# Kernel optimization log

Hardware: AMD Instinct MI355X
Metric: run time of the kernel (lower is better)

## Reference

```python
import jax, jax.numpy as jnp
import numpy as np

NUM_HEADS = 8
BLOCK_SIZE = 32   # tokens per block
WINDOW = 64       # window radius in blocks -> attends to blocks [i-64, i+64]


def setup_inputs() -> dict:
    key = jax.random.key(0)
    ks = jax.random.split(key, 5)
    B, N, C = 8, 8192, 512
    s = 0.02
    return {
        "x": jax.random.normal(ks[0], (B, N, C), dtype=jnp.float32),
        # torch Linear(dim, 3*dim): y = x @ W.T + b; we store W already transposed [in, out]
        "W_qkv": jax.random.normal(ks[1], (C, 3 * C), dtype=jnp.float32) * s,
        "b_qkv": jax.random.normal(ks[2], (3 * C,), dtype=jnp.float32) * s,
        "W_proj": jax.random.normal(ks[3], (C, C), dtype=jnp.float32) * s,
        "b_proj": jax.random.normal(ks[4], (C,), dtype=jnp.float32) * s,
    }


def reference(x, W_qkv, b_qkv, W_proj, b_proj):
    B, N, C = x.shape
    h = NUM_HEADS
    dh = C // h
    scale = jnp.asarray(dh, x.dtype) ** -0.5

    # qkv projection, then the module's head-interleaved split:
    # rearrange 'b n (h d) -> b h n d' with d = 3C/h, chunk(3) on last dim,
    # rearrange back 'b h n d -> b n (h d)'. Equivalent to:
    qkv = (x @ W_qkv + b_qkv).reshape(B, N, h, 3 * dh)
    q = qkv[..., :dh].reshape(B, N, C)
    k = qkv[..., dh:2 * dh].reshape(B, N, C)
    v = qkv[..., 2 * dh:].reshape(B, N, C)

    # dynamic blocking (N chosen divisible by BLOCK_SIZE -> no padding)
    nb = N // BLOCK_SIZE
    qb = q.reshape(B, nb, BLOCK_SIZE, C)
    kb = k.reshape(B, nb, BLOCK_SIZE, C)
    vb = v.reshape(B, nb, BLOCK_SIZE, C)

    # per-offset block attention: query block i, position s attends to
    # position s of every block j in [i-WINDOW, i+WINDOW]
    attn = jnp.einsum('bisc,bjsc->bisj', qb, kb) * scale  # [B, nb, s, nb]
    i_idx = jnp.arange(nb)[:, None]
    j_idx = jnp.arange(nb)[None, :]
    band = (j_idx >= i_idx - WINDOW) & (j_idx <= i_idx + WINDOW)  # [nb, nb]
    neg = jnp.finfo(attn.dtype).min
    attn = jnp.where(band[None, :, None, :], attn, neg)
    attn = jax.nn.softmax(attn, axis=-1)
    out = jnp.einsum('bisj,bjsc->bisc', attn, vb)  # [B, nb, s, C]
    out = out.reshape(B, N, C)

    # 'b n (h d) -> b n h d -> b n (h d)' is the identity
    return out @ W_proj + b_proj
```

## Files before the change

kernel.cpp:

```cpp
#include <hip/hip_runtime.h>
#include <hip/hip_bf16.h>
#include <stdint.h>

#define B_   8
#define N_   8192
#define C_   512
#define NB   256
#define WIN  64

typedef __attribute__((ext_vector_type(8))) short short8;
typedef __attribute__((ext_vector_type(4))) float f32x4;
typedef __hip_bfloat16 bf16;

__device__ __forceinline__ void gload_lds16(const void* g, void* l) {
  __builtin_amdgcn_global_load_lds((const __attribute__((address_space(1))) void*)g,
                                   (__attribute__((address_space(3))) void*)l, 16, 0, 0);
}

__device__ __forceinline__ f32x4 mfma16(short8 a, short8 b, f32x4 c) {
  return __builtin_amdgcn_mfma_f32_16x16x32_bf16(a, b, c, 0, 0, 0);
}


__global__ __launch_bounds__(256) void k_conv_x(const float4* __restrict__ x,
                                                ushort4* __restrict__ xb) {
  size_t idx = (size_t)blockIdx.x * 256 + threadIdx.x;
  float4 v = x[idx];
  union { ushort4 u; bf16 b[4]; } o;
  o.b[0] = __float2bfloat16(v.x); o.b[1] = __float2bfloat16(v.y);
  o.b[2] = __float2bfloat16(v.z); o.b[3] = __float2bfloat16(v.w);
  xb[idx] = o.u;
}

__global__ __launch_bounds__(256) void k_conv_wqkv(const float* __restrict__ W,
                                                   const float* __restrict__ bq,
                                                   bf16* __restrict__ Wt,
                                                   float* __restrict__ bperm) {
  int o = blockIdx.x;
  int part = o >> 9;
  int c = o & 511;
  int h = c >> 6, d = c & 63;
  int src = h * 192 + part * 64 + d;
  for (int kk = threadIdx.x; kk < 512; kk += 256)
    Wt[(size_t)o * 512 + kk] = __float2bfloat16(W[(size_t)kk * 1536 + src]);
  if (threadIdx.x == 0) bperm[o] = bq[src];
}

__global__ __launch_bounds__(256) void k_conv_wproj(const float* __restrict__ W,
                                                    bf16* __restrict__ Wt) {
  int o = blockIdx.x;
  for (int kk = threadIdx.x; kk < 512; kk += 256)
    Wt[(size_t)o * 512 + kk] = __float2bfloat16(W[(size_t)kk * 512 + o]);
}

template <int EPI>
__global__ __launch_bounds__(512, 2) void k_gemm(const bf16* __restrict__ A,
                                                 const bf16* __restrict__ Bt,
                                                 const float* __restrict__ bias,
                                                 bf16* __restrict__ qb,
                                                 bf16* __restrict__ kb,
                                                 bf16* __restrict__ vb,
                                                 float* __restrict__ outf,
                                                 int NT) {
  extern __shared__ bf16 sm[];
  const int tid = threadIdx.x;
  const int lane = tid & 63, wid = tid >> 6;
  const int wr = wid >> 2, wcn = wid & 3;
  const int l15 = lane & 15, l4 = lane >> 4;

  const int nwg = gridDim.x;
  const int cpx = nwg >> 3;
  const int swz = (blockIdx.x & 7) * cpx + (blockIdx.x >> 3);
  const int mt = swz / NT, nt = swz % NT;
  const size_t m0 = (size_t)mt * 256;
  const int n0 = nt * 256;

  f32x4 acc[8][4];
#pragma unroll
  for (int fi = 0; fi < 8; ++fi)
#pragma unroll
    for (int fj = 0; fj < 4; ++fj) acc[fi][fj] = (f32x4){0.f, 0.f, 0.f, 0.f};

#define STAGEG(slot, k0)                                                       \
  {                                                                            \
    bf16* Adst = sm + (slot) * 32768;                                          \
    bf16* Bdst = Adst + 16384;                                                 \
    _Pragma("unroll") for (int i = 0; i < 4; ++i) {                            \
      int li = i * 512 + tid;                                                  \
      int row = li >> 3, ch = li & 7;                                          \
      int chs = ch ^ (row & 7);                                                \
      gload_lds16(A + (m0 + row) * 512 + (k0) + chs * 8,                       \
                  (char*)Adst + li * 16);                                      \
      gload_lds16(Bt + (size_t)(n0 + row) * 512 + (k0) + chs * 8,              \
                  (char*)Bdst + li * 16);                                      \
    }                                                                          \
  }

  STAGEG(0, 0);
  for (int t = 0; t < 8; ++t) {
    if (t < 7) {
      STAGEG((t + 1) & 1, (t + 1) * 64);
      asm volatile("s_waitcnt vmcnt(8)" ::: "memory");
    } else {
      asm volatile("s_waitcnt vmcnt(0)" ::: "memory");
    }
    __builtin_amdgcn_s_barrier();
    __builtin_amdgcn_sched_barrier(0);
    const bf16* Ap = sm + (t & 1) * 32768;
    const bf16* Bp = Ap + 16384;
#pragma unroll
    for (int ks = 0; ks < 2; ++ks) {
      short8 a[8], b[4];
#pragma unroll
      for (int fi = 0; fi < 8; ++fi) {
        int ra = wr * 128 + fi * 16 + l15;
        a[fi] = *(const short8*)&Ap[ra * 64 + (((ks * 4 + l4) ^ (ra & 7)) << 3)];
      }
#pragma unroll
      for (int fj = 0; fj < 4; ++fj) {
        int rb = wcn * 64 + fj * 16 + l15;
        b[fj] = *(const short8*)&Bp[rb * 64 + (((ks * 4 + l4) ^ (rb & 7)) << 3)];
      }
      __builtin_amdgcn_s_setprio(1);
#pragma unroll
      for (int fi = 0; fi < 8; ++fi)
#pragma unroll
        for (int fj = 0; fj < 4; ++fj)
          acc[fi][fj] = mfma16(a[fi], b[fj], acc[fi][fj]);
      __builtin_amdgcn_s_setprio(0);
    }
    __builtin_amdgcn_sched_barrier(0);
    __builtin_amdgcn_s_barrier();
  }
#undef STAGEG

  if (EPI == 0) {
#pragma unroll
    for (int fi = 0; fi < 8; ++fi)
#pragma unroll
      for (int fj = 0; fj < 4; ++fj) {
        int o = n0 + wcn * 64 + fj * 16 + l15;
        float bia = bias[o];
        int part = o >> 9;
        int c = o & 511;
        bf16* dst = part == 0 ? qb : (part == 1 ? kb : vb);
#pragma unroll
        for (int r = 0; r < 4; ++r) {
          size_t m = m0 + wr * 128 + fi * 16 + l4 * 4 + r;
          int bidx = (int)(m >> 13);
          int n = (int)(m & 8191);
          int blk = n >> 5, s = n & 31;
          size_t di = (((size_t)(bidx * 32 + s) * 256 + blk) << 9) | c;
          dst[di] = __float2bfloat16(acc[fi][fj][r] + bia);
        }
      }
  } else {
#pragma unroll
    for (int fi = 0; fi < 8; ++fi)
#pragma unroll
      for (int fj = 0; fj < 4; ++fj) {
        int o = n0 + wcn * 64 + fj * 16 + l15;
        float bia = bias[o];
#pragma unroll
        for (int r = 0; r < 4; ++r) {
          size_t m = m0 + wr * 128 + fi * 16 + l4 * 4 + r;
          outf[m * 512 + o] = acc[fi][fj][r] + bia;
        }
      }
  }
}

__global__ __launch_bounds__(256) void k_transpose_v(const bf16* __restrict__ v,
                                                     bf16* __restrict__ vT) {
  __shared__ bf16 t[32][36];
  int bs = blockIdx.x, j0 = blockIdx.y * 32, c0 = blockIdx.z * 32;
  const bf16* src = v + (size_t)bs * NB * C_;
  bf16* dst = vT + (size_t)bs * C_ * NB;
  int r = threadIdx.x >> 3, c4 = (threadIdx.x & 7) * 4;
  *(ushort4*)&t[r][c4] = *(const ushort4*)(src + (size_t)(j0 + r) * C_ + c0 + c4);
  __syncthreads();
  union { ushort4 u; bf16 b[4]; } o;
  o.b[0] = t[c4 + 0][r]; o.b[1] = t[c4 + 1][r];
  o.b[2] = t[c4 + 2][r]; o.b[3] = t[c4 + 3][r];
  *(ushort4*)(dst + (size_t)(c0 + r) * NB + j0 + c4) = o.u;
}

#define QS_OFF   0
#define KB_OFF   32768
#define VB_OFF   98304
#define SS_OFF   131072
#define PS_OFF   135296
#define SR_OFF   137856
#define MR_OFF   141952
#define LR_OFF   142080
#define AL_OFF   142208
#define ATTN_LDS 142336

__global__ __launch_bounds__(512) void k_attn(const bf16* __restrict__ qg,
                                              const bf16* __restrict__ kg,
                                              const bf16* __restrict__ vTg,
                                              bf16* __restrict__ outb) {
  extern __shared__ char smc[];
  float* Ssf  = (float*)(smc + SS_OFF);
  bf16*  Psb  = (bf16*)(smc + PS_OFF);
  float* Sred = (float*)(smc + SR_OFF);
  float* mrow = (float*)(smc + MR_OFF);
  float* lrow = (float*)(smc + LR_OFF);
  float* alph = (float*)(smc + AL_OFF);

  const int tid = threadIdx.x, lane = tid & 63, wid = tid >> 6;
  const int l15 = lane & 15, l4 = lane >> 4;
  const int gt = (blockIdx.x & 7) * 256 + (blockIdx.x >> 3);
  const int bs = gt >> 3;
  const int b = bs >> 5, s = bs & 31;
  const int i0 = (gt & 7) * 32;
  const int jlo = max(0, i0 - WIN);
  const int jhi = min(NB - 1, i0 + 31 + WIN);
  const int nch = (jhi - jlo + 1) >> 5;
  const bf16* Qb = qg + (size_t)bs * NB * C_;
  const bf16* Kb = kg + (size_t)bs * NB * C_;
  const bf16* Vb = vTg + (size_t)bs * C_ * NB;

  const int qh_qk = (wid >> 2) & 1, jh = (wid >> 1) & 1, ks = wid & 1;
  const int qh_pv = wid >> 2, cq = wid & 3;

  f32x4 O[8];
#pragma unroll
  for (int f = 0; f < 8; ++f) O[f] = (f32x4){0.f, 0.f, 0.f, 0.f};

  if (tid < 32) { mrow[tid] = -1e30f; lrow[tid] = 0.f; }

#pragma unroll
  for (int q = 0; q < 4; ++q) {
    int li = q * 512 + tid;
    int row = li >> 6, g = (li & 63) ^ (row & 15);
    gload_lds16(Qb + (size_t)(i0 + row) * C_ + g * 8, smc + QS_OFF + li * 16);
  }
#pragma unroll
  for (int q = 0; q < 4; ++q) {
    int li = q * 512 + tid;
    int row = li >> 6, g = (li & 63) ^ (row & 15);
    gload_lds16(Kb + (size_t)(jlo + row) * C_ + g * 8, smc + KB_OFF + li * 16);
  }

  for (int t = 0; t < nch; ++t) {
    const int j0 = jlo + t * 32;
    asm volatile("s_waitcnt vmcnt(0) lgkmcnt(0)" ::: "memory");
    __builtin_amdgcn_s_barrier();
    __builtin_amdgcn_sched_barrier(0);

#pragma unroll
    for (int q = 0; q < 4; ++q) {
      int li = q * 512 + tid;
      int c = li >> 2, g = (li & 3) ^ (c & 3);
      gload_lds16(Vb + (size_t)c * NB + j0 + g * 8, smc + VB_OFF + li * 16);
    }
    if (t + 1 < nch) {
      int jn = j0 + 32;
      char* kdst = smc + KB_OFF + ((t + 1) & 1) * 32768;
#pragma unroll
      for (int q = 0; q < 4; ++q) {
        int li = q * 512 + tid;
        int row = li >> 6, g = (li & 63) ^ (row & 15);
        gload_lds16(Kb + (size_t)(jn + row) * C_ + g * 8, kdst + li * 16);
      }
    }

    {
      const int arow = qh_qk * 16 + l15;
      const int brow = jh * 16 + l15;
      const char* Qbase = smc + QS_OFF + arow * 1024;
      const char* Kbase = smc + KB_OFF + (t & 1) * 32768 + brow * 1024;
      f32x4 a0 = (f32x4){0.f, 0.f, 0.f, 0.f}, a1 = a0;
      __builtin_amdgcn_s_setprio(1);
#pragma unroll
      for (int cc = 0; cc < 8; ++cc) {
        int sa = (ks * 32 + cc * 4 + l4) ^ (arow & 15);
        int sb = (ks * 32 + cc * 4 + l4) ^ (brow & 15);
        short8 av = *(const short8*)(Qbase + sa * 16);
        short8 bv = *(const short8*)(Kbase + sb * 16);
        if (cc & 1) a1 = mfma16(av, bv, a1);
        else        a0 = mfma16(av, bv, a0);
      }
      __builtin_amdgcn_s_setprio(0);
      f32x4 acc = a0 + a1;
      if (ks) {
        *(f32x4*)&Sred[(wid >> 1) * 256 + lane * 4] = acc;
      }
      asm volatile("s_waitcnt lgkmcnt(0)" ::: "memory");
      __builtin_amdgcn_s_barrier();
      __builtin_amdgcn_sched_barrier(0);
      if (!ks) {
        f32x4 su = acc + *(f32x4*)&Sred[(wid >> 1) * 256 + lane * 4];
        int jg = j0 + jh * 16 + l15;
#pragma unroll
        for (int r = 0; r < 4; ++r) {
          int i_in = qh_qk * 16 + l4 * 4 + r;
          int i_abs = i0 + i_in;
          bool valid = (jg >= i_abs - WIN) && (jg <= i_abs + WIN);
          Ssf[i_in * 33 + jh * 16 + l15] = valid ? su[r] * 0.125f : -1e30f;
        }
      }
      asm volatile("s_waitcnt lgkmcnt(0)" ::: "memory");
      __builtin_amdgcn_s_barrier();
      __builtin_amdgcn_sched_barrier(0);
    }

    {
      int row = tid >> 4, u = tid & 15;
      float s0 = Ssf[row * 33 + u], s1 = Ssf[row * 33 + u + 16];
      float mc = fmaxf(s0, s1);
      mc = fmaxf(mc, __shfl_xor(mc, 1));
      mc = fmaxf(mc, __shfl_xor(mc, 2));
      mc = fmaxf(mc, __shfl_xor(mc, 4));
      mc = fmaxf(mc, __shfl_xor(mc, 8));
      float mo = mrow[row];
      float mn = fmaxf(mo, mc);
      float a = __expf(mo - mn);
      float p0 = __expf(s0 - mn), p1 = __expf(s1 - mn);
      float ps = p0 + p1;
      ps += __shfl_xor(ps, 1);
      ps += __shfl_xor(ps, 2);
      ps += __shfl_xor(ps, 4);
      ps += __shfl_xor(ps, 8);
      if (u == 0) {
        lrow[row] = lrow[row] * a + ps;
        mrow[row] = mn;
        alph[row] = a;
      }
      Psb[row * 40 + u] = __float2bfloat16(p0);
      Psb[row * 40 + u + 16] = __float2bfloat16(p1);
    }
    if (t + 1 < nch)
      asm volatile("s_waitcnt vmcnt(4) lgkmcnt(0)" ::: "memory");
    else
      asm volatile("s_waitcnt vmcnt(0) lgkmcnt(0)" ::: "memory");
    __builtin_amdgcn_s_barrier();
    __builtin_amdgcn_sched_barrier(0);

    {
      float ar[4];
#pragma unroll
      for (int r = 0; r < 4; ++r) ar[r] = alph[qh_pv * 16 + l4 * 4 + r];
      short8 pa = *(const short8*)(smc + PS_OFF + (qh_pv * 16 + l15) * 80 + l4 * 16);
      __builtin_amdgcn_s_setprio(1);
#pragma unroll
      for (int f = 0; f < 8; ++f) {
        int c = cq * 128 + f * 16 + l15;
        short8 vv = *(const short8*)(smc + VB_OFF + c * 64 + ((l4 ^ (c & 3)) << 4));
#pragma unroll
        for (int r = 0; r < 4; ++r) O[f][r] *= ar[r];
        O[f] = mfma16(pa, vv, O[f]);
      }
      __builtin_amdgcn_s_setprio(0);
    }
    __builtin_amdgcn_sched_barrier(0);
  }

  asm volatile("s_waitcnt lgkmcnt(0)" ::: "memory");
  __builtin_amdgcn_s_barrier();
  {
    float lr[4];
#pragma unroll
    for (int r = 0; r < 4; ++r) lr[r] = 1.f / lrow[qh_pv * 16 + l4 * 4 + r];
#pragma unroll
    for (int f = 0; f < 8; ++f) {
      int c = cq * 128 + f * 16 + l15;
#pragma unroll
      for (int r = 0; r < 4; ++r) {
        int il = qh_pv * 16 + l4 * 4 + r;
        int n = (i0 + il) * 32 + s;
        outb[((size_t)b * N_ + n) * C_ + c] = __float2bfloat16(O[f][r] * lr[r]);
      }
    }
  }
}

extern "C" void kernel_launch(void* const* d_in, const int* in_sizes, int n_in,
                              void* d_out, int out_size, void* d_ws, size_t ws_size,
                              hipStream_t stream) {
  const float* x = (const float*)d_in[0];
  const float* Wqkv = (const float*)d_in[1];
  const float* bqkv = (const float*)d_in[2];
  const float* Wproj = (const float*)d_in[3];
  const float* bproj = (const float*)d_in[4];

  char* ws = (char*)d_ws;
  const size_t SLOT = 67108864ull;
  bf16* slotA = (bf16*)ws;
  bf16* slotB = (bf16*)(ws + SLOT);
  bf16* Wqkv_t = (bf16*)(ws + 2 * SLOT);
  bf16* Wproj_t = (bf16*)(ws + 2 * SLOT + 1572864);
  float* bias_perm = (float*)(ws + 2 * SLOT + 1572864 + 524288);
  bf16* qbuf = (bf16*)d_out;
  bf16* kbuf = qbuf + 33554432ull;

  static int attr_done = 0;
  if (!attr_done) {
    hipFuncSetAttribute((const void*)k_gemm<0>,
                        hipFuncAttributeMaxDynamicSharedMemorySize, 131072);
    hipFuncSetAttribute((const void*)k_gemm<1>,
                        hipFuncAttributeMaxDynamicSharedMemorySize, 131072);
    hipFuncSetAttribute((const void*)k_attn,
                        hipFuncAttributeMaxDynamicSharedMemorySize, ATTN_LDS);
    attr_done = 1;
  }

  k_conv_x<<<32768, 256, 0, stream>>>((const float4*)x, (ushort4*)slotA);
  k_conv_wqkv<<<1536, 256, 0, stream>>>(Wqkv, bqkv, Wqkv_t, bias_perm);
  k_conv_wproj<<<512, 256, 0, stream>>>(Wproj, Wproj_t);

  k_gemm<0><<<256 * 6, 512, 131072, stream>>>(slotA, Wqkv_t, bias_perm,
                                              qbuf, kbuf, slotB, nullptr, 6);
  k_transpose_v<<<dim3(256, 8, 16), 256, 0, stream>>>(slotB, slotA);
  k_attn<<<2048, 512, ATTN_LDS, stream>>>(qbuf, kbuf, slotA, slotB);
  k_gemm<1><<<256 * 2, 512, 131072, stream>>>(slotB, Wproj_t, bproj,
                                              nullptr, nullptr, nullptr, (float*)d_out, 2);
}
```

Before: 339.1 us.

## Split GEMM K-step into four quadrant phases with interleaved half-tile prefetch

Restructures the bf16 GEMM main loop so each 64-wide K step runs as four phases over A/B half-tiles. Each phase issues the global-to-LDS load for one half-tile of the next stage, with finer vmcnt waits and barriers between phases, so prefetch overlaps with MFMA work at a finer grain. The warp-to-fragment mapping changes to an interleaved layout (rows fi*32+wr*16, cols fj*64+wcn*16), which smaller per-phase register sets need. In exchange it adds more barriers per K step and relies on hand-counted vmcnt values, which is fragile.

```diff
diff --git a/kernel.cpp b/kernel.cpp
--- a/kernel.cpp
+++ b/kernel.cpp
@@ -53,6 +53,8 @@
     Wt[(size_t)o * 512 + kk] = __float2bfloat16(W[(size_t)kk * 512 + o]);
 }
 
+#define WAITV(N) asm volatile("s_waitcnt vmcnt(" #N ")" ::: "memory")
+
 template <int EPI>
 __global__ __launch_bounds__(512, 2) void k_gemm(const bf16* __restrict__ A,
                                                  const bf16* __restrict__ Bt,
@@ -62,11 +64,12 @@
                                                  bf16* __restrict__ vb,
                                                  float* __restrict__ outf,
                                                  int NT) {
-  extern __shared__ bf16 sm[];
+  extern __shared__ char gsm[];
   const int tid = threadIdx.x;
   const int lane = tid & 63, wid = tid >> 6;
   const int wr = wid >> 2, wcn = wid & 3;
   const int l15 = lane & 15, l4 = lane >> 4;
+  const int sx = l15 & 7;
 
   const int nwg = gridDim.x;
   const int cpx = nwg >> 3;
@@ -81,72 +84,93 @@
 #pragma unroll
     for (int fj = 0; fj < 4; ++fj) acc[fi][fj] = (f32x4){0.f, 0.f, 0.f, 0.f};
 
-#define STAGEG(slot, k0)                                                       \
+#define STAGE_A(E, H, K0)                                                      \
+  { _Pragma("unroll") for (int q = 0; q < 2; ++q) {                            \
+      int li = q * 512 + tid;                                                  \
+      int r = li >> 3, g = (li & 7) ^ (r & 7);                                 \
+      gload_lds16(A + (m0 + (H) * 128 + r) * 512 + (K0) + g * 8,               \
+                  gsm + (E) * 65536 + (H) * 16384 + li * 16);                  \
+    } }
+#define STAGE_B(E, H, K0)                                                      \
+  { _Pragma("unroll") for (int q = 0; q < 2; ++q) {                            \
+      int li = q * 512 + tid;                                                  \
+      int r = li >> 3, g = (li & 7) ^ (r & 7);                                 \
+      gload_lds16(Bt + (size_t)(n0 + (H) * 128 + r) * 512 + (K0) + g * 8,      \
+                  gsm + (E) * 65536 + 32768 + (H) * 16384 + li * 16);          \
+    } }
+
+#define PHASE(FIH, FJH, LOADA, STAGE_STMT, WAIT_STMT)                          \
   {                                                                            \
-    bf16* Adst = sm + (slot) * 32768;                                          \
-    bf16* Bdst = Adst + 16384;                                                 \
-    _Pragma("unroll") for (int i = 0; i < 4; ++i) {                            \
-      int li = i * 512 + tid;                                                  \
-      int row = li >> 3, ch = li & 7;                                          \
-      int chs = ch ^ (row & 7);                                                \
-      gload_lds16(A + (m0 + row) * 512 + (k0) + chs * 8,                       \
-                  (char*)Adst + li * 16);                                      \
-      gload_lds16(Bt + (size_t)(n0 + row) * 512 + (k0) + chs * 8,              \
-                  (char*)Bdst + li * 16);                                      \
+    const char* Ab = gsm + d * 65536 + (FIH) * 16384;                          \
+    const char* Bb = gsm + d * 65536 + 32768 + (FJH) * 16384;                  \
+    if (LOADA) {                                                               \
+      _Pragma("unroll") for (int f = 0; f < 4; ++f) {                          \
+        int rA = f * 32 + wr * 16 + l15;                                       \
+        af[f][0] = *(const short8*)(Ab + rA * 128 + ((l4 ^ sx) << 4));         \
+        af[f][1] = *(const short8*)(Ab + rA * 128 + (((4 + l4) ^ sx) << 4));   \
+      }                                                                        \
     }                                                                          \
-  }
-
-  STAGEG(0, 0);
+    _Pragma("unroll") for (int f = 0; f < 2; ++f) {                            \
+      int rB = f * 64 + wcn * 16 + l15;                                        \
+      bfr[f][0] = *(const short8*)(Bb + rB * 128 + ((l4 ^ sx) << 4));          \
+      bfr[f][1] = *(const short8*)(Bb + rB * 128 + (((4 + l4) ^ sx) << 4));    \
+    }                                                                          \
+    STAGE_STMT;                                                                \
+    __builtin_amdgcn_sched_barrier(0);                                         \
+    __builtin_amdgcn_s_barrier();                                              \
+    __builtin_amdgcn_sched_barrier(0);                                         \
+    __builtin_amdgcn_s_setprio(1);                                             \
+    _Pragma("unroll") for (int f = 0; f < 4; ++f)                              \
+      _Pragma("unroll") for (int g = 0; g < 2; ++g) {                          \
+        acc[(FIH) * 4 + f][(FJH) * 2 + g] =                                    \
+            mfma16(af[f][0], bfr[g][0], acc[(FIH) * 4 + f][(FJH) * 2 + g]);    \
+        acc[(FIH) * 4 + f][(FJH) * 2 + g] =                                    \
+            mfma16(af[f][1], bfr[g][1], acc[(FIH) * 4 + f][(FJH) * 2 + g]);    \
+      }                                                                        \
+    __builtin_amdgcn_s_setprio(0);                                             \
+    __builtin_amdgcn_sched_barrier(0);                                         \
+    WAIT_STMT;                                                                 \
+    __builtin_amdgcn_s_barrier();                                              \
+  }
+
+  STAGE_A(0, 0, 0); STAGE_B(0, 0, 0); STAGE_B(0, 1, 0); STAGE_A(0, 1, 0);
+  WAITV(4);
+  __builtin_amdgcn_s_barrier();
+
+  short8 af[4][2], bfr[2][2];
   for (int t = 0; t < 8; ++t) {
-    if (t < 7) {
-      STAGEG((t + 1) & 1, (t + 1) * 64);
-      asm volatile("s_waitcnt vmcnt(8)" ::: "memory");
-    } else {
-      asm volatile("s_waitcnt vmcnt(0)" ::: "memory");
-    }
-    __builtin_amdgcn_s_barrier();
-    __builtin_amdgcn_sched_barrier(0);
-    const bf16* Ap = sm + (t & 1) * 32768;
-    const bf16* Bp = Ap + 16384;
-#pragma unroll
-    for (int ks = 0; ks < 2; ++ks) {
-      short8 a[8], b[4];
-#pragma unroll
-      for (int fi = 0; fi < 8; ++fi) {
-        int ra = wr * 128 + fi * 16 + l15;
-        a[fi] = *(const short8*)&Ap[ra * 64 + (((ks * 4 + l4) ^ (ra & 7)) << 3)];
-      }
+    const int d = t & 1, e = d ^ 1;
+    const int kn = (t + 1) * 64;
+    PHASE(0, 0, 1,
+          { if (t < 7) STAGE_A(e, 0, kn); },
+          { if (t < 7) { WAITV(4); } else { WAITV(2); } });
+    PHASE(0, 1, 0,
+          { if (t < 7) STAGE_B(e, 0, kn); },
+          { if (t < 7) { WAITV(4); } else { WAITV(0); } });
+    PHASE(1, 0, 1,
+          { if (t < 7) STAGE_B(e, 1, kn); },
+          { });
+    PHASE(1, 1, 0,
+          { if (t < 7) STAGE_A(e, 1, kn); },
+          { if (t < 7) { WAITV(4); } });
+  }
+#undef PHASE
+#undef STAGE_A
+#undef STAGE_B
+
+  if (EPI == 0) {
+#pragma unroll
+    for (int fi = 0; fi < 8; ++fi)
 #pragma unroll
       for (int fj = 0; fj < 4; ++fj) {
-        int rb = wcn * 64 + fj * 16 + l15;
-        b[fj] = *(const short8*)&Bp[rb * 64 + (((ks * 4 + l4) ^ (rb & 7)) << 3)];
-      }
-      __builtin_amdgcn_s_setprio(1);
-#pragma unroll
-      for (int fi = 0; fi < 8; ++fi)
-#pragma unroll
-        for (int fj = 0; fj < 4; ++fj)
-          acc[fi][fj] = mfma16(a[fi], b[fj], acc[fi][fj]);
-      __builtin_amdgcn_s_setprio(0);
-    }
-    __builtin_amdgcn_sched_barrier(0);
-    __builtin_amdgcn_s_barrier();
-  }
-#undef STAGEG
-
-  if (EPI == 0) {
-#pragma unroll
-    for (int fi = 0; fi < 8; ++fi)
-#pragma unroll
-      for (int fj = 0; fj < 4; ++fj) {
-        int o = n0 + wcn * 64 + fj * 16 + l15;
+        int o = n0 + fj * 64 + wcn * 16 + l15;
         float bia = bias[o];
         int part = o >> 9;
         int c = o & 511;
         bf16* dst = part == 0 ? qb : (part == 1 ? kb : vb);
 #pragma unroll
         for (int r = 0; r < 4; ++r) {
-          size_t m = m0 + wr * 128 + fi * 16 + l4 * 4 + r;
+          size_t m = m0 + fi * 32 + wr * 16 + l4 * 4 + r;
           int bidx = (int)(m >> 13);
           int n = (int)(m & 8191);
           int blk = n >> 5, s = n & 31;
@@ -159,11 +183,11 @@
     for (int fi = 0; fi < 8; ++fi)
 #pragma unroll
       for (int fj = 0; fj < 4; ++fj) {
-        int o = n0 + wcn * 64 + fj * 16 + l15;
+        int o = n0 + fj * 64 + wcn * 16 + l15;
         float bia = bias[o];
 #pragma unroll
         for (int r = 0; r < 4; ++r) {
-          size_t m = m0 + wr * 128 + fi * 16 + l4 * 4 + r;
+          size_t m = m0 + fi * 32 + wr * 16 + l4 * 4 + r;
           outf[m * 512 + o] = acc[fi][fj][r] + bia;
         }
       }
@@ -410,10 +434,10 @@
   k_conv_wqkv<<<1536, 256, 0, stream>>>(Wqkv, bqkv, Wqkv_t, bias_perm);
   k_conv_wproj<<<512, 256, 0, stream>>>(Wproj, Wproj_t);
 
-  k_gemm<0><<<256 * 6, 512, 131072, stream>>>(slotA, Wqkv_t, bias_perm,
-                                              qbuf, kbuf, slotB, nullptr, 6);
+  k_gemm<0><<<1536, 512, 131072, stream>>>(slotA, Wqkv_t, bias_perm,
+                                           qbuf, kbuf, slotB, nullptr, 6);
   k_transpose_v<<<dim3(256, 8, 16), 256, 0, stream>>>(slotB, slotA);
   k_attn<<<2048, 512, ATTN_LDS, stream>>>(qbuf, kbuf, slotA, slotB);
-  k_gemm<1><<<256 * 2, 512, 131072, stream>>>(slotB, Wproj_t, bproj,
-                                              nullptr, nullptr, nullptr, (float*)d_out, 2);
-}
+  k_gemm<1><<<512, 512, 131072, stream>>>(slotB, Wproj_t, bproj,
+                                          nullptr, nullptr, nullptr, (float*)d_out, 2);
+}
```

Measured after the change: 337.1 us. No clear change (-0.6%).
